# Performance work log

Hardware: AMD Instinct MI355X
Metric: run time of the kernel (lower is better)

The kernel has to match this reference:

```python
import jax, jax.numpy as jnp
import numpy as np

B, S, D, H = 4, 2048, 1024, 16
DH = D // H  # 64


def setup_inputs() -> dict:
    key = jax.random.key(0)
    ks = jax.random.split(key, 11)
    s = 0.02
    return {
        "query": jax.random.normal(ks[0], (B, S, D), jnp.float32),
        "key": jax.random.normal(ks[1], (B, S, D), jnp.float32),
        "value": jax.random.normal(ks[2], (B, S, D), jnp.float32),
        "Wq": jax.random.normal(ks[3], (D, D), jnp.float32) * s,
        "bq": jnp.zeros((D,), jnp.float32),
        "Wk": jax.random.normal(ks[4], (D, D), jnp.float32) * s,
        "bk": jnp.zeros((D,), jnp.float32),
        "Wv": jax.random.normal(ks[5], (D, D), jnp.float32) * s,
        "bv": jnp.zeros((D,), jnp.float32),
        "Wo": jax.random.normal(ks[6], (D, D), jnp.float32) * s,
        "bo": jnp.zeros((D,), jnp.float32),
    }


def reference(query, key, value, Wq, bq, Wk, bk, Wv, bv, Wo, bo):
    b, s, _ = query.shape
    # linear projections (torch Linear: x @ W^T + b; here W stored as [in, out])
    q = query @ Wq + bq
    k = key @ Wk + bk
    v = value @ Wv + bv
    # split heads -> [B, H, S, DH]
    q = q.reshape(b, s, H, DH).transpose(0, 2, 1, 3)
    k = k.reshape(b, s, H, DH).transpose(0, 2, 1, 3)
    v = v.reshape(b, s, H, DH).transpose(0, 2, 1, 3)
    scale = jnp.sqrt(jnp.asarray(DH, jnp.float32))
    attn = jnp.einsum("bhqd,bhkd->bhqk", q, k) / scale  # [B,H,S,S]
    attn = jax.nn.softmax(attn, axis=-1)
    out = jnp.einsum("bhqk,bhkd->bhqd", attn, v)
    out = out.transpose(0, 2, 1, 3).reshape(b, s, D)
    return out @ Wo + bo
```

## Files before the change

### kernel.cpp

```cpp
#include <hip/hip_runtime.h>

typedef float f32x4 __attribute__((ext_vector_type(4)));
typedef __bf16 bf16x8 __attribute__((ext_vector_type(8)));
typedef unsigned short u16;
typedef unsigned int u32;
typedef u16 u16x4 __attribute__((ext_vector_type(4)));
typedef u16 u16x8 __attribute__((ext_vector_type(8)));
typedef u32 u32x2 __attribute__((ext_vector_type(2)));
typedef u32 u32x4 __attribute__((ext_vector_type(4)));

constexpr int Bn = 4, Sn = 2048, Dn = 1024, Hn = 16, DHn = 64;
constexpr int Mn = Bn * Sn;

static __device__ __forceinline__ u16 f2bf(float f) {
  return __builtin_bit_cast(u16, (__bf16)f);
}

static __device__ __forceinline__ u32 cvtpk(float lo, float hi) {
  u32 r;
  asm("v_cvt_pk_bf16_f32 %0, %1, %2" : "=v"(r) : "v"(lo), "v"(hi));
  return r;
}

static __device__ __forceinline__ void async16(const void* g, void* l) {
  __builtin_amdgcn_global_load_lds((const __attribute__((address_space(1))) u32*)g,
                                   (__attribute__((address_space(3))) u32*)l, 16, 0, 0);
}

static __device__ __forceinline__ void wait_bar2() {
  asm volatile("s_waitcnt vmcnt(2)" ::: "memory");
  __builtin_amdgcn_sched_barrier(0);
  __builtin_amdgcn_s_barrier();
  __builtin_amdgcn_sched_barrier(0);
}
static __device__ __forceinline__ void wait_bar8() {
  asm volatile("s_waitcnt vmcnt(8)" ::: "memory");
  __builtin_amdgcn_sched_barrier(0);
  __builtin_amdgcn_s_barrier();
  __builtin_amdgcn_sched_barrier(0);
}
static __device__ __forceinline__ void wait_bar0() {
  asm volatile("s_waitcnt vmcnt(0)" ::: "memory");
  __builtin_amdgcn_sched_barrier(0);
  __builtin_amdgcn_s_barrier();
  __builtin_amdgcn_sched_barrier(0);
}
static __device__ __forceinline__ void raw_bar() {
  __builtin_amdgcn_sched_barrier(0);
  __builtin_amdgcn_s_barrier();
  __builtin_amdgcn_sched_barrier(0);
}
static __device__ __forceinline__ void qkv_wait4() {
  asm volatile("s_waitcnt vmcnt(4) lgkmcnt(0)" ::: "memory");
  __builtin_amdgcn_sched_barrier(0);
  __builtin_amdgcn_s_barrier();
  __builtin_amdgcn_sched_barrier(0);
}
static __device__ __forceinline__ void qkv_wait0() {
  asm volatile("s_waitcnt vmcnt(0) lgkmcnt(0)" ::: "memory");
  __builtin_amdgcn_sched_barrier(0);
  __builtin_amdgcn_s_barrier();
  __builtin_amdgcn_sched_barrier(0);
}

__global__ void __launch_bounds__(256) transpose4_kernel(const float* __restrict__ Wq,
                                                         const float* __restrict__ Wk,
                                                         const float* __restrict__ Wv,
                                                         const float* __restrict__ Wo,
                                                         u16* __restrict__ Wts) {
  __shared__ float tile[32][33];
  const int z = blockIdx.z;
  const float* W = (z == 0) ? Wq : (z == 1) ? Wk : (z == 2) ? Wv : Wo;
  u16* Wt = Wts + (size_t)z * Dn * Dn;
  const int n0 = blockIdx.x * 32, k0 = blockIdx.y * 32;
  const int tx = threadIdx.x & 31, ty = (threadIdx.x >> 5) * 4;
#pragma unroll
  for (int i = 0; i < 4; ++i)
    tile[ty + i][tx] = W[(size_t)(k0 + ty + i) * Dn + n0 + tx];
  __syncthreads();
#pragma unroll
  for (int i = 0; i < 4; ++i)
    Wt[(size_t)(n0 + ty + i) * Dn + k0 + tx] = f2bf(tile[tx][ty + i]);
}

__global__ void __launch_bounds__(256) gemm_qkv_kernel(const float* __restrict__ q_in,
                                                       const float* __restrict__ k_in,
                                                       const float* __restrict__ v_in,
                                                       const u16* __restrict__ Wts,
                                                       const float* __restrict__ bq,
                                                       const float* __restrict__ bk,
                                                       const float* __restrict__ bv,
                                                       u16* __restrict__ outbase) {
  __shared__ u16 As[2][128 * 64];
  __shared__ u16 Bs[3][128 * 64];

  const int bid = blockIdx.x;
  const int xcd = bid & 7;
  const int loc = bid >> 3;
  const int nb = loc & 7;
  const int panel = xcd * 24 + (loc >> 3);
  const int z = panel >> 6;
  const int m0 = (panel & 63) * 128, n0 = nb * 128;

  const float* A = (z == 0) ? q_in : (z == 1) ? k_in : v_in;
  const u16* Bt = Wts + (size_t)z * Dn * Dn;
  const float* bias = (z == 0) ? bq : (z == 1) ? bk : bv;
  u16* outp = outbase + (size_t)z * Mn * Dn;
  const float scale = (z == 0) ? 0.125f * 1.4426950408889634f : 1.0f;

  const int tid = threadIdx.x;
  const int wave = tid >> 6, lane = tid & 63;
  const int g = lane >> 4, c = lane & 15;
  const int wm = wave >> 1, wn = wave & 1;
  const int srow = lane >> 3, blk = lane & 7;

  f32x4 acc[4][4] = {};
  constexpr int NK = Dn / 64;

  f32x4 rA0lo[4], rA0hi[4], rA1lo[4], rA1hi[4];

  auto issueA = [&](int k0, f32x4 (&rlo)[4], f32x4 (&rhi)[4]) {
#pragma unroll
    for (int i = 0; i < 4; ++i) {
      const int row = (wave * 4 + i) * 8 + srow;
      const float* src = A + (size_t)(m0 + row) * Dn + k0 + blk * 8;
      rlo[i] = *(const f32x4*)src;
      rhi[i] = *(const f32x4*)(src + 4);
    }
  };
  auto writeA = [&](u16* dst, f32x4 (&rlo)[4], f32x4 (&rhi)[4]) {
#pragma unroll
    for (int i = 0; i < 4; ++i) {
      const int row = (wave * 4 + i) * 8 + srow;
      u32x4 w;
      w[0] = cvtpk(rlo[i][0], rlo[i][1]);
      w[1] = cvtpk(rlo[i][2], rlo[i][3]);
      w[2] = cvtpk(rhi[i][0], rhi[i][1]);
      w[3] = cvtpk(rhi[i][2], rhi[i][3]);
      *(u32x4*)(dst + row * 64 + ((blk ^ srow) * 8)) = w;
    }
  };
  auto issueB = [&](int k0, u16* dstB) {
#pragma unroll
    for (int i = 0; i < 4; ++i) {
      const int ch = wave * 4 + i, row = ch * 8 + srow, sb = blk ^ srow;
      async16(Bt + (size_t)(n0 + row) * Dn + k0 + sb * 8, dstB + ch * 512);
    }
  };
  auto mfma_tile = [&](const u16* Asb, const u16* Bsb) {
#pragma unroll
    for (int kk = 0; kk < 2; ++kk) {
      bf16x8 af[4], bfr[4];
#pragma unroll
      for (int mi = 0; mi < 4; ++mi)
        af[mi] = *(const bf16x8*)(Asb + (wm * 64 + mi * 16 + c) * 64 +
                                  (((kk * 4 + g) ^ (c & 7)) * 8));
#pragma unroll
      for (int ni = 0; ni < 4; ++ni)
        bfr[ni] = *(const bf16x8*)(Bsb + (wn * 64 + ni * 16 + c) * 64 +
                                   (((kk * 4 + g) ^ (c & 7)) * 8));
      __builtin_amdgcn_s_setprio(1);
#pragma unroll
      for (int mi = 0; mi < 4; ++mi)
#pragma unroll
        for (int ni = 0; ni < 4; ++ni)
          acc[mi][ni] = __builtin_amdgcn_mfma_f32_16x16x32_bf16(af[mi], bfr[ni],
                                                                acc[mi][ni], 0, 0, 0);
      __builtin_amdgcn_s_setprio(0);
    }
  };

  u16 *bA = Bs[0], *bB = Bs[1], *bC = Bs[2];

  issueA(0, rA0lo, rA0hi);
  issueB(0, bA);
  asm volatile("s_waitcnt vmcnt(4)" ::: "memory");
  __builtin_amdgcn_sched_barrier(0);
  writeA(As[0], rA0lo, rA0hi);
  issueA(64, rA1lo, rA1hi);
  issueB(64, bB);

  for (int kp = 0; kp < NK; kp += 2) {
    {
      const int t = kp;
      if (t + 1 < NK) qkv_wait4(); else qkv_wait0();
      if (t + 2 < NK) {
        issueA((t + 2) * 64, rA0lo, rA0hi);
        issueB((t + 2) * 64, bC);
      }
      if (t + 1 < NK) writeA(As[1], rA1lo, rA1hi);
      mfma_tile(As[0], bA);
      u16* tb = bA; bA = bB; bB = bC; bC = tb;
    }
    {
      const int t = kp + 1;
      if (t + 1 < NK) qkv_wait4(); else qkv_wait0();
      if (t + 2 < NK) {
        issueA((t + 2) * 64, rA1lo, rA1hi);
        issueB((t + 2) * 64, bC);
      }
      if (t + 1 < NK) writeA(As[0], rA0lo, rA0hi);
      mfma_tile(As[1], bA);
      u16* tb = bA; bA = bB; bB = bC; bC = tb;
    }
  }

  const bool vmode = (z == 2);
#pragma unroll
  for (int ni = 0; ni < 4; ++ni) {
    const int col = n0 + wn * 64 + ni * 16 + c;
    const float bv = bias[col];
    const int hh = col >> 6, dh = col & 63;
#pragma unroll
    for (int mi = 0; mi < 4; ++mi) {
      const int row = m0 + wm * 64 + mi * 16 + g * 4;
      const int bb = row >> 11, s = row & 2047;
      if (!vmode) {
        u16* o = outp + (((size_t)(bb * Hn + hh) * Sn + s) * DHn + dh);
#pragma unroll
        for (int r = 0; r < 4; ++r)
          o[(size_t)r * DHn] = f2bf((acc[mi][ni][r] + bv) * scale);
      } else {
        u16x4 pk;
#pragma unroll
        for (int r = 0; r < 4; ++r) pk[r] = f2bf(acc[mi][ni][r] + bv);
        *(u16x4*)(outp + ((size_t)(bb * Hn + hh) * DHn + dh) * Sn + s) = pk;
      }
    }
  }
}

__global__ void __launch_bounds__(256) gemm_o_kernel(const u16* __restrict__ A,
                                                     const u16* __restrict__ Bt,
                                                     const float* __restrict__ bias,
                                                     float* __restrict__ outp) {
  __shared__ u16 As[2][128 * 64];
  __shared__ u16 Bs[2][128 * 64];
  const int bid = blockIdx.x;
  const int xcd = bid & 7;
  const int loc = bid >> 3;
  const int nb = loc & 7;
  const int panel = xcd * 8 + (loc >> 3);
  const int m0 = panel * 128, n0 = nb * 128;

  const int tid = threadIdx.x;
  const int wave = tid >> 6, lane = tid & 63;
  const int g = lane >> 4, c = lane & 15;
  const int wm = wave >> 1, wn = wave & 1;
  const int srow = lane >> 3, blk = lane & 7;

  f32x4 acc[4][4] = {};
  constexpr int NK = Dn / 64;

#pragma unroll
  for (int p = 0; p < 2; ++p) {
    const int k0 = p * 64;
#pragma unroll
    for (int i = 0; i < 4; ++i) {
      const int ch = wave * 4 + i;
      const int row = ch * 8 + srow;
      const int sblk = blk ^ srow;
      async16(A + (size_t)(m0 + row) * Dn + k0 + sblk * 8, As[p] + ch * 512);
      async16(Bt + (size_t)(n0 + row) * Dn + k0 + sblk * 8, Bs[p] + ch * 512);
    }
  }

  for (int k = 0; k < NK; ++k) {
    const int cur = k & 1;
    if (k + 1 < NK) wait_bar8(); else wait_bar0();

#pragma unroll
    for (int kk = 0; kk < 2; ++kk) {
      bf16x8 af[4], bfr[4];
#pragma unroll
      for (int mi = 0; mi < 4; ++mi)
        af[mi] = *(const bf16x8*)(As[cur] + (wm * 64 + mi * 16 + c) * 64 +
                                  (((kk * 4 + g) ^ (c & 7)) * 8));
#pragma unroll
      for (int ni = 0; ni < 4; ++ni)
        bfr[ni] = *(const bf16x8*)(Bs[cur] + (wn * 64 + ni * 16 + c) * 64 +
                                   (((kk * 4 + g) ^ (c & 7)) * 8));
#pragma unroll
      for (int mi = 0; mi < 4; ++mi)
#pragma unroll
        for (int ni = 0; ni < 4; ++ni)
          acc[mi][ni] = __builtin_amdgcn_mfma_f32_16x16x32_bf16(af[mi], bfr[ni],
                                                                acc[mi][ni], 0, 0, 0);
    }

    raw_bar();
    if (k + 2 < NK) {
      const int k0 = (k + 2) * 64;
#pragma unroll
      for (int i = 0; i < 4; ++i) {
        const int ch = wave * 4 + i;
        const int row = ch * 8 + srow;
        const int sblk = blk ^ srow;
        async16(A + (size_t)(m0 + row) * Dn + k0 + sblk * 8, As[cur] + ch * 512);
        async16(Bt + (size_t)(n0 + row) * Dn + k0 + sblk * 8, Bs[cur] + ch * 512);
      }
    }
  }

#pragma unroll
  for (int ni = 0; ni < 4; ++ni) {
    const int col = n0 + wn * 64 + ni * 16 + c;
    const float bv = bias[col];
#pragma unroll
    for (int mi = 0; mi < 4; ++mi) {
      const int row = m0 + wm * 64 + mi * 16 + g * 4;
      float* o = outp + (size_t)row * Dn + col;
#pragma unroll
      for (int r = 0; r < 4; ++r) o[(size_t)r * Dn] = acc[mi][ni][r] + bv;
    }
  }
}

__global__ void __launch_bounds__(512, 4) attn_kernel(const u16* __restrict__ Q,
                                                      const u16* __restrict__ Kp,
                                                      const u16* __restrict__ VT,
                                                      u16* __restrict__ O) {
  __shared__ u16 Ks[3][64 * 64];
  __shared__ u16 Vs[3][64 * 64];
  const int tid = threadIdx.x;
  const int wave = tid >> 6, lane = tid & 63;
  const int g = lane >> 4, c = lane & 15;
  const int bh = blockIdx.x;
  const int q0 = blockIdx.y * 256 + wave * 32;
  const u16* Qb = Q + (size_t)bh * Sn * DHn;
  const u16* Kb = Kp + (size_t)bh * Sn * DHn;
  const u16* Vb = VT + (size_t)bh * DHn * Sn;

  bf16x8 qf[2][2];
#pragma unroll
  for (int fq = 0; fq < 2; ++fq)
#pragma unroll
    for (int kk = 0; kk < 2; ++kk)
      qf[fq][kk] = *(const bf16x8*)(Qb + (size_t)(q0 + fq * 16 + c) * DHn + kk * 32 + g * 8);

  f32x4 ot[4][2] = {};
  f32x4 lacc[2] = {};
  u16x8 one8u;
#pragma unroll
  for (int j = 0; j < 8; ++j) one8u[j] = 0x3F80;
  const bf16x8 one8 = __builtin_bit_cast(bf16x8, one8u);
  const f32x4 zf = {};

  const int srow = lane >> 3, blk = lane & 7;
  const int krow = wave * 8 + srow;
  const int sblk = blk ^ srow;
  constexpr int NT = Sn / 64;

  u16 *kA = Ks[0], *kB = Ks[1], *kC = Ks[2];
  u16 *vA = Vs[0], *vB = Vs[1], *vC = Vs[2];

#pragma unroll
  for (int tt = 0; tt < 2; ++tt) {
    const int kt = tt * 64;
    async16(Kb + (size_t)(kt + krow) * DHn + sblk * 8, Ks[tt] + wave * 512);
    async16(Vb + (size_t)krow * Sn + kt + sblk * 8, Vs[tt] + wave * 512);
  }

  for (int t = 0; t < NT; ++t) {
    if (t + 1 < NT) wait_bar2(); else wait_bar0();

    if (t + 2 < NT) {
      const int kt = (t + 2) * 64;
      async16(Kb + (size_t)(kt + krow) * DHn + sblk * 8, kC + wave * 512);
      async16(Vb + (size_t)krow * Sn + kt + sblk * 8, vC + wave * 512);
    }

    f32x4 st[4][2];
    {
      bf16x8 kf[4];
#pragma unroll
      for (int fk = 0; fk < 4; ++fk)
        kf[fk] = *(const bf16x8*)(kA + (fk * 16 + c) * 64 + ((g ^ (c & 7)) * 8));
      __builtin_amdgcn_s_setprio(1);
#pragma unroll
      for (int fk = 0; fk < 4; ++fk)
#pragma unroll
        for (int fq = 0; fq < 2; ++fq)
          st[fk][fq] = __builtin_amdgcn_mfma_f32_16x16x32_bf16(kf[fk], qf[fq][0],
                                                               zf, 0, 0, 0);
      __builtin_amdgcn_s_setprio(0);
#pragma unroll
      for (int fk = 0; fk < 4; ++fk)
        kf[fk] = *(const bf16x8*)(kA + (fk * 16 + c) * 64 + (((4 + g) ^ (c & 7)) * 8));
      __builtin_amdgcn_s_setprio(1);
#pragma unroll
      for (int fk = 0; fk < 4; ++fk)
#pragma unroll
        for (int fq = 0; fq < 2; ++fq)
          st[fk][fq] = __builtin_amdgcn_mfma_f32_16x16x32_bf16(kf[fk], qf[fq][1],
                                                               st[fk][fq], 0, 0, 0);
      __builtin_amdgcn_s_setprio(0);
    }

#pragma unroll
    for (int fq = 0; fq < 2; ++fq)
#pragma unroll
      for (int fk = 0; fk < 4; ++fk)
#pragma unroll
        for (int r = 0; r < 4; ++r)
          st[fk][fq][r] = __builtin_amdgcn_exp2f(st[fk][fq][r]);

    bf16x8 pf[2][2];
#pragma unroll
    for (int fq = 0; fq < 2; ++fq)
#pragma unroll
      for (int kk = 0; kk < 2; ++kk) {
        u32x4 pw;
#pragma unroll
        for (int w = 0; w < 2; ++w) {
          const u32 a = cvtpk(st[2 * kk][fq][2 * w], st[2 * kk][fq][2 * w + 1]);
          const u32 b = cvtpk(st[2 * kk + 1][fq][2 * w], st[2 * kk + 1][fq][2 * w + 1]);
          const u32x2 p1 = __builtin_amdgcn_permlane32_swap(a, b, false, false);
          const u32x2 p2 = __builtin_amdgcn_permlane16_swap(p1[0], p1[1], false, false);
          pw[w] = p2[0];
          pw[2 + w] = p2[1];
        }
        pf[kk][fq] = __builtin_bit_cast(bf16x8, pw);
      }

#pragma unroll
    for (int kk = 0; kk < 2; ++kk) {
      bf16x8 vf[4];
#pragma unroll
      for (int fa = 0; fa < 4; ++fa)
        vf[fa] = *(const bf16x8*)(vA + (fa * 16 + c) * 64 +
                                  (((kk * 4 + g) ^ (c & 7)) * 8));
      __builtin_amdgcn_s_setprio(1);
#pragma unroll
      for (int fa = 0; fa < 4; ++fa)
#pragma unroll
        for (int fq = 0; fq < 2; ++fq)
          ot[fa][fq] = __builtin_amdgcn_mfma_f32_16x16x32_bf16(vf[fa], pf[kk][fq],
                                                               ot[fa][fq], 0, 0, 0);
#pragma unroll
      for (int fq = 0; fq < 2; ++fq)
        lacc[fq] = __builtin_amdgcn_mfma_f32_16x16x32_bf16(one8, pf[kk][fq],
                                                           lacc[fq], 0, 0, 0);
      __builtin_amdgcn_s_setprio(0);
    }

    u16* tk = kA; kA = kB; kB = kC; kC = tk;
    u16* tv = vA; vA = vB; vB = vC; vC = tv;
  }

  const int bb = bh >> 4, hh = bh & 15;
#pragma unroll
  for (int fq = 0; fq < 2; ++fq) {
    const float inv = 1.f / lacc[fq][0];
    const int s = q0 + fq * 16 + c;
#pragma unroll
    for (int fa = 0; fa < 4; ++fa) {
      const int dh = fa * 16 + g * 4;
      u16x4 pk;
#pragma unroll
      for (int r = 0; r < 4; ++r) pk[r] = f2bf(ot[fa][fq][r] * inv);
      *(u16x4*)(O + ((size_t)bb * Sn + s) * Dn + hh * 64 + dh) = pk;
    }
  }
}

extern "C" void kernel_launch(void* const* d_in, const int* in_sizes, int n_in,
                              void* d_out, int out_size, void* d_ws, size_t ws_size,
                              hipStream_t stream) {
  (void)in_sizes; (void)n_in; (void)out_size; (void)ws_size;
  const float* q_in = (const float*)d_in[0];
  const float* k_in = (const float*)d_in[1];
  const float* v_in = (const float*)d_in[2];
  const float* Wq = (const float*)d_in[3];
  const float* bq = (const float*)d_in[4];
  const float* Wk = (const float*)d_in[5];
  const float* bk = (const float*)d_in[6];
  const float* Wv = (const float*)d_in[7];
  const float* bv = (const float*)d_in[8];
  const float* Wo = (const float*)d_in[9];
  const float* bo = (const float*)d_in[10];

  char* ws = (char*)d_ws;
  const size_t szX = (size_t)Mn * Dn * 2;
  const size_t szW = (size_t)Dn * Dn * 2;
  u16* Wts = (u16*)ws;
  u16* Qb = (u16*)(ws + 4 * szW + 0 * szX);
  u16* Kb = (u16*)(ws + 4 * szW + 1 * szX);
  u16* VTb = (u16*)(ws + 4 * szW + 2 * szX);
  u16* Ob = (u16*)(ws + 4 * szW + 3 * szX);

  transpose4_kernel<<<dim3(32, 32, 4), 256, 0, stream>>>(Wq, Wk, Wv, Wo, Wts);

  gemm_qkv_kernel<<<1536, 256, 0, stream>>>(q_in, k_in, v_in, Wts, bq, bk, bv, Qb);

  attn_kernel<<<dim3(Bn * Hn, Sn / 256), 512, 0, stream>>>(Qb, Kb, VTb, Ob);

  gemm_o_kernel<<<512, 256, 0, stream>>>(Ob, Wts + (size_t)3 * Dn * Dn, bo,
                                         (float*)d_out);
}
```

Baseline: 173.1 us.

## Software-pipeline attention loop so QK of next tile overlaps PV of previous

Restructures the attention main loop so that each iteration runs the QK^T MFMAs for the current tile, then the PV MFMAs for the previous tile's probabilities, then the exp and pack for the current tile. The aim is to let the exp and permlane conversions overlap with independent MFMA work instead of sitting on the dependency chain. A fourth V shared-memory buffer keeps the previous tile's V resident, and two ping-ponged probability register sets carry results across iterations. This raises LDS and register use, which may reduce occupancy.

```diff
diff --git a/kernel.cpp b/kernel.cpp
--- a/kernel.cpp
+++ b/kernel.cpp
@@ -321,7 +321,7 @@
                                                       const u16* __restrict__ VT,
                                                       u16* __restrict__ O) {
   __shared__ u16 Ks[3][64 * 64];
-  __shared__ u16 Vs[3][64 * 64];
+  __shared__ u16 Vs[4][64 * 64];
   const int tid = threadIdx.x;
   const int wave = tid >> 6, lane = tid & 63;
   const int g = lane >> 4, c = lane & 15;
@@ -352,7 +352,7 @@
   constexpr int NT = Sn / 64;
 
   u16 *kA = Ks[0], *kB = Ks[1], *kC = Ks[2];
-  u16 *vA = Vs[0], *vB = Vs[1], *vC = Vs[2];
+  u16 *vP = Vs[3], *vA = Vs[0], *vB = Vs[1], *vC = Vs[2];
 
 #pragma unroll
   for (int tt = 0; tt < 2; ++tt) {
@@ -361,42 +361,58 @@
     async16(Vb + (size_t)krow * Sn + kt + sblk * 8, Vs[tt] + wave * 512);
   }
 
-  for (int t = 0; t < NT; ++t) {
-    if (t + 1 < NT) wait_bar2(); else wait_bar0();
-
-    if (t + 2 < NT) {
-      const int kt = (t + 2) * 64;
-      async16(Kb + (size_t)(kt + krow) * DHn + sblk * 8, kC + wave * 512);
-      async16(Vb + (size_t)krow * Sn + kt + sblk * 8, vC + wave * 512);
-    }
-
-    f32x4 st[4][2];
-    {
-      bf16x8 kf[4];
-#pragma unroll
-      for (int fk = 0; fk < 4; ++fk)
-        kf[fk] = *(const bf16x8*)(kA + (fk * 16 + c) * 64 + ((g ^ (c & 7)) * 8));
+  bf16x8 pfA[2][2] = {}, pfB[2][2] = {};
+
+  auto do_qk = [&](f32x4 (&st)[4][2]) {
+    bf16x8 kf[4];
+#pragma unroll
+    for (int fk = 0; fk < 4; ++fk)
+      kf[fk] = *(const bf16x8*)(kA + (fk * 16 + c) * 64 + ((g ^ (c & 7)) * 8));
+    __builtin_amdgcn_s_setprio(1);
+#pragma unroll
+    for (int fk = 0; fk < 4; ++fk)
+#pragma unroll
+      for (int fq = 0; fq < 2; ++fq)
+        st[fk][fq] = __builtin_amdgcn_mfma_f32_16x16x32_bf16(kf[fk], qf[fq][0],
+                                                             zf, 0, 0, 0);
+    __builtin_amdgcn_s_setprio(0);
+#pragma unroll
+    for (int fk = 0; fk < 4; ++fk)
+      kf[fk] = *(const bf16x8*)(kA + (fk * 16 + c) * 64 + (((4 + g) ^ (c & 7)) * 8));
+    __builtin_amdgcn_s_setprio(1);
+#pragma unroll
+    for (int fk = 0; fk < 4; ++fk)
+#pragma unroll
+      for (int fq = 0; fq < 2; ++fq)
+        st[fk][fq] = __builtin_amdgcn_mfma_f32_16x16x32_bf16(kf[fk], qf[fq][1],
+                                                             st[fk][fq], 0, 0, 0);
+    __builtin_amdgcn_s_setprio(0);
+  };
+
+  auto do_pv = [&](const bf16x8 (&pfv)[2][2]) {
+#pragma unroll
+    for (int kk = 0; kk < 2; ++kk) {
+      bf16x8 vf[4];
+#pragma unroll
+      for (int fa = 0; fa < 4; ++fa)
+        vf[fa] = *(const bf16x8*)(vP + (fa * 16 + c) * 64 +
+                                  (((kk * 4 + g) ^ (c & 7)) * 8));
       __builtin_amdgcn_s_setprio(1);
 #pragma unroll
-      for (int fk = 0; fk < 4; ++fk)
+      for (int fa = 0; fa < 4; ++fa)
 #pragma unroll
         for (int fq = 0; fq < 2; ++fq)
-          st[fk][fq] = __builtin_amdgcn_mfma_f32_16x16x32_bf16(kf[fk], qf[fq][0],
-                                                               zf, 0, 0, 0);
+          ot[fa][fq] = __builtin_amdgcn_mfma_f32_16x16x32_bf16(vf[fa], pfv[kk][fq],
+                                                               ot[fa][fq], 0, 0, 0);
+#pragma unroll
+      for (int fq = 0; fq < 2; ++fq)
+        lacc[fq] = __builtin_amdgcn_mfma_f32_16x16x32_bf16(one8, pfv[kk][fq],
+                                                           lacc[fq], 0, 0, 0);
       __builtin_amdgcn_s_setprio(0);
-#pragma unroll
-      for (int fk = 0; fk < 4; ++fk)
-        kf[fk] = *(const bf16x8*)(kA + (fk * 16 + c) * 64 + (((4 + g) ^ (c & 7)) * 8));
-      __builtin_amdgcn_s_setprio(1);
-#pragma unroll
-      for (int fk = 0; fk < 4; ++fk)
-#pragma unroll
-        for (int fq = 0; fq < 2; ++fq)
-          st[fk][fq] = __builtin_amdgcn_mfma_f32_16x16x32_bf16(kf[fk], qf[fq][1],
-                                                               st[fk][fq], 0, 0, 0);
-      __builtin_amdgcn_s_setprio(0);
-    }
-
+    }
+  };
+
+  auto do_sm = [&](f32x4 (&st)[4][2], bf16x8 (&pfo)[2][2]) {
 #pragma unroll
     for (int fq = 0; fq < 2; ++fq)
 #pragma unroll
@@ -404,8 +420,6 @@
 #pragma unroll
         for (int r = 0; r < 4; ++r)
           st[fk][fq][r] = __builtin_amdgcn_exp2f(st[fk][fq][r]);
-
-    bf16x8 pf[2][2];
 #pragma unroll
     for (int fq = 0; fq < 2; ++fq)
 #pragma unroll
@@ -420,33 +434,36 @@
           pw[w] = p2[0];
           pw[2 + w] = p2[1];
         }
-        pf[kk][fq] = __builtin_bit_cast(bf16x8, pw);
+        pfo[kk][fq] = __builtin_bit_cast(bf16x8, pw);
       }
-
-#pragma unroll
-    for (int kk = 0; kk < 2; ++kk) {
-      bf16x8 vf[4];
-#pragma unroll
-      for (int fa = 0; fa < 4; ++fa)
-        vf[fa] = *(const bf16x8*)(vA + (fa * 16 + c) * 64 +
-                                  (((kk * 4 + g) ^ (c & 7)) * 8));
-      __builtin_amdgcn_s_setprio(1);
-#pragma unroll
-      for (int fa = 0; fa < 4; ++fa)
-#pragma unroll
-        for (int fq = 0; fq < 2; ++fq)
-          ot[fa][fq] = __builtin_amdgcn_mfma_f32_16x16x32_bf16(vf[fa], pf[kk][fq],
-                                                               ot[fa][fq], 0, 0, 0);
-#pragma unroll
-      for (int fq = 0; fq < 2; ++fq)
-        lacc[fq] = __builtin_amdgcn_mfma_f32_16x16x32_bf16(one8, pf[kk][fq],
-                                                           lacc[fq], 0, 0, 0);
-      __builtin_amdgcn_s_setprio(0);
-    }
-
+  };
+
+  auto rotate = [&]() {
     u16* tk = kA; kA = kB; kB = kC; kC = tk;
-    u16* tv = vA; vA = vB; vB = vC; vC = tv;
-  }
+    u16* tv = vP; vP = vA; vA = vB; vB = vC; vC = tv;
+  };
+
+  auto body = [&](int t, const bf16x8 (&pfIn)[2][2], bf16x8 (&pfOut)[2][2],
+                  bool doPV) {
+    if (t + 1 < NT) wait_bar2(); else wait_bar0();
+    if (t + 2 < NT) {
+      const int kt = (t + 2) * 64;
+      async16(Kb + (size_t)(kt + krow) * DHn + sblk * 8, kC + wave * 512);
+      async16(Vb + (size_t)krow * Sn + kt + sblk * 8, vC + wave * 512);
+    }
+    f32x4 st[4][2];
+    do_qk(st);
+    if (doPV) do_pv(pfIn);
+    do_sm(st, pfOut);
+    rotate();
+  };
+
+  body(0, pfB, pfA, false);
+  for (int tp = 1; tp < NT; tp += 2) {
+    body(tp, pfA, pfB, true);
+    if (tp + 1 < NT) body(tp + 1, pfB, pfA, true);
+  }
+  do_pv(pfB);
 
   const int bb = bh >> 4, hh = bh & 15;
 #pragma unroll
```

Result: slower. 194.0 us (+12.1%).
